# Kernel tuning notes

Measured on AMD Instinct MI355X. Metric: run time of the kernel, lower is better.

The kernel has to match this reference:

```python
import jax, jax.numpy as jnp
import numpy as np

DX = 0.01
DT = 0.5
MU_UP = 0.001

_lap = np.array([[0,0,-1/12,0,0],[0,0,4/3,0,0],[-1/12,4/3,-5,4/3,-1/12],[0,0,4/3,0,0],[0,0,-1/12,0,0]], dtype=np.float32)
_dx = np.array([[0,0,1/12,0,0],[0,0,-8/12,0,0],[0,0,0,0,0],[0,0,8/12,0,0],[0,0,-1/12,0,0]], dtype=np.float32)
K_LAP = jnp.asarray(_lap)[None, None] / (DX * DX)   # [1,1,5,5]
K_DX = jnp.asarray(_dx)[None, None] / DX             # derivative along H axis (torch res_dx)
K_DY = jnp.swapaxes(K_DX, 2, 3)                      # derivative along W axis (torch res_dy)


def _conv(x, k):
    # cross-correlation, VALID, NCHW -- matches torch Conv2d
    return jax.lax.conv_general_dilated(x, k, (1, 1), 'VALID',
                                        dimension_numbers=('NCHW', 'OIHW', 'NCHW'))


def _pad(h):
    # periodic padding of 2 on both spatial dims (torch.cat based circular pad)
    return jnp.pad(h, ((0, 0), (0, 0), (2, 2), (2, 2)), mode='wrap')


def _f_rhs(u, v, Re, UA, UB, VA, VB):
    up, vp = _pad(u), _pad(v)
    u_x, u_y = _conv(up, K_DX), _conv(up, K_DY)
    v_x, v_y = _conv(vp, K_DX), _conv(vp, K_DY)
    nu = MU_UP / Re
    f_u = nu * _conv(up, K_LAP) + UA * u * u_x + UB * v * u_y
    f_v = nu * _conv(vp, K_LAP) + VA * u * v_x + VB * v * v_y
    return f_u, f_v


def setup_inputs() -> dict:
    key = jax.random.key(0)
    k_h, k_re, k_ua, k_ub, k_va, k_vb = jax.random.split(key, 6)
    h = jax.random.normal(k_h, (8, 2, 1024, 1024), dtype=jnp.float32)
    Re = jax.random.uniform(k_re, (), jnp.float32, 0.5, 1.5)  # keep 1/Re well-conditioned
    UA = jax.random.uniform(k_ua, (), jnp.float32)
    UB = jax.random.uniform(k_ub, (), jnp.float32)
    VA = jax.random.uniform(k_va, (), jnp.float32)
    VB = jax.random.uniform(k_vb, (), jnp.float32)
    return {'h': h, 'Re': Re, 'UA': UA, 'UB': UB, 'VA': VA, 'VB': VB}


def reference(h, Re, UA, UB, VA, VB):
    u0 = h[:, 0:1]
    v0 = h[:, 1:2]
    k1u, k1v = _f_rhs(u0, v0, Re, UA, UB, VA, VB)
    k2u, k2v = _f_rhs(u0 + k1u * (DT / 2.0), v0 + k1v * (DT / 2.0), Re, UA, UB, VA, VB)
    k3u, k3v = _f_rhs(u0 + k2u * (DT / 2.0), v0 + k2v * (DT / 2.0), Re, UA, UB, VA, VB)
    k4u, k4v = _f_rhs(u0 + k3u * DT, v0 + k3v * DT, Re, UA, UB, VA, VB)
    u_next = u0 + DT * (k1u + 2 * k2u + 2 * k3u + k4u) / 6.0
    v_next = v0 + DT * (k1v + 2 * k2v + 2 * k3v + k4v) / 6.0
    return jnp.concatenate((u_next, v_next), axis=1)
```

## Files before the change

### kernel.cpp

```cpp
#include <hip/hip_runtime.h>


typedef float f4 __attribute__((ext_vector_type(4)));
typedef float f2 __attribute__((ext_vector_type(2)));

#define LCOLS 100
#define NFLD  8192
#define NT    1024

#define GLOAD16(gp, lp) __builtin_amdgcn_global_load_lds(                      \
    (const __attribute__((address_space(1))) void*)(gp),                       \
    (__attribute__((address_space(3))) void*)(lp), 16, 0, 0)

template<int S>
__device__ __forceinline__ void quad_stage(
    const float* tu, const float* tv, int l,
    float nu, float UA, float UB, float VA, float VB,
    f4& ku, f4& kv, f4& au, f4& av, f4& su, f4& sv, f4& ou, f4& ov)
{
    const float csub = (S==0) ? 0.f : ((S==3) ? 0.5f : 0.25f);
    const float cadd = (S<=1) ? 0.25f : ((S==2) ? 0.5f : 0.f);
    const float wgt  = (S==1 || S==2) ? 2.f : 1.f;
    const float d1 = 800.f/12.f;
    const float d2 = 100.f/12.f;
    const float a1 = (4.f/3.f)*1.0e4f;
    const float a2 = -(1.f/12.f)*1.0e4f;
    const float a0 = -5.0e4f;

    f4 ucc, vcc;
    if (S == 0) { ucc = *(const f4*)(tu+l); vcc = *(const f4*)(tv+l); }
    else        { ucc = su;                 vcc = sv; }
    f2 ul2 = *(const f2*)(tu+l-2);
    f2 ur2 = *(const f2*)(tu+l+4);
    f4 un1 = *(const f4*)(tu+l-LCOLS);
    f4 us1 = *(const f4*)(tu+l+LCOLS);
    f4 un2 = *(const f4*)(tu+l-2*LCOLS);
    f4 us2 = *(const f4*)(tu+l+2*LCOLS);
    f2 vl2 = *(const f2*)(tv+l-2);
    f2 vr2 = *(const f2*)(tv+l+4);
    f4 vn1 = *(const f4*)(tv+l-LCOLS);
    f4 vs1 = *(const f4*)(tv+l+LCOLS);
    f4 vn2 = *(const f4*)(tv+l-2*LCOLS);
    f4 vs2 = *(const f4*)(tv+l+2*LCOLS);
    float hu[8] = {ul2[0],ul2[1],ucc[0],ucc[1],ucc[2],ucc[3],ur2[0],ur2[1]};
    float hv[8] = {vl2[0],vl2[1],vcc[0],vcc[1],vcc[2],vcc[3],vr2[0],vr2[1]};
#pragma unroll
    for (int k = 0; k < 4; ++k) {
        float u = hu[k+2], v = hv[k+2];
        float urow = d1*(us1[k]-un1[k]) + d2*(un2[k]-us2[k]);
        float vrow = d1*(vs1[k]-vn1[k]) + d2*(vn2[k]-vs2[k]);
        float ucol = d1*(hu[k+3]-hu[k+1]) + d2*(hu[k]-hu[k+4]);
        float vcol = d1*(hv[k+3]-hv[k+1]) + d2*(hv[k]-hv[k+4]);
        float ulap = a1*((un1[k]+us1[k])+(hu[k+1]+hu[k+3]))
                   + a2*((un2[k]+us2[k])+(hu[k]+hu[k+4])) + a0*u;
        float vlap = a1*((vn1[k]+vs1[k])+(hv[k+1]+hv[k+3]))
                   + a2*((vn2[k]+vs2[k])+(hv[k]+hv[k+4])) + a0*v;
        float fu = nu*ulap + UA*(u*urow) + UB*(v*ucol);
        float fv = nu*vlap + VA*(u*vrow) + VB*(v*vcol);
        float kuold = ku[k], kvold = kv[k];
        if (S == 3) {
            ou[k] = (u - 0.5f*kuold) + (1.f/12.f)*(au[k] + fu);
            ov[k] = (v - 0.5f*kvold) + (1.f/12.f)*(av[k] + fv);
        } else {
            au[k] += wgt*fu;
            av[k] += wgt*fv;
            su[k] = (u - csub*kuold) + cadd*fu;
            sv[k] = (v - csub*kvold) + cadd*fv;
            ku[k] = fu;
            kv[k] = fv;
        }
    }
}

__global__ __launch_bounds__(NT, 4)
void rk4_stencil(const float* __restrict__ h,
                 const float* __restrict__ sRe, const float* __restrict__ sUA,
                 const float* __restrict__ sUB, const float* __restrict__ sVA,
                 const float* __restrict__ sVB, float* __restrict__ out)
{
    __shared__ __align__(16) float tu[NFLD];
    __shared__ __align__(16) float tv[NFLD];

    const int tid = threadIdx.x;
    const int tc = blockIdx.x, tr = blockIdx.y, bb = blockIdx.z;

    const float Re = sRe[0], UA = sUA[0], UB = sUB[0], VA = sVA[0], VB = sVB[0];
    const float nu = 0.001f / Re;
    const f4 z4 = {0.f, 0.f, 0.f, 0.f};

    const size_t plane = 1048576;
    const float* uin = h + (size_t)(bb*2) * plane;
    const float* vin = uin + plane;
    const int base_r = tr*64 - 8  + 1024;
    const int base_c = tc*64 - 16 + 1024;

    {
        const int wave = tid >> 6, lane = tid & 63;
#pragma unroll
        for (int it = 0; it < 4; ++it) {
            int c = wave + 16*it;
            int fld = (c >= 32);
            int cc  = c & 31;
            int idx = 256*cc + 4*lane;
            int row = idx / LCOLS;
            int col = idx - row*LCOLS;
            int gr = (base_r + row) & 1023;
            int gc = (base_c + col) & 1023;
            const float* gp = (fld ? vin : uin) + ((size_t)gr << 10) + gc;
            float* lp = (fld ? tv : tu) + 256*cc;
            GLOAD16(gp, lp);
        }
    }
    __syncthreads();

    const int wv = tid >> 6, ln = tid & 63;
    const int dqr = 8 + 4*wv + (ln >> 4);
    const int dqc = 4 + (ln & 15);
    const int dl  = dqr*LCOLS + 4*dqc;

    int rqr = 0, rqc = 0;
    if (tid < 496) {
        int i = tid;
        if      (i < 36)  { rqr = 6  + i/18;       rqc = 3 + i%18; }
        else if (i < 72)  { int t=i-36;  rqr = 72 + t/18; rqc = 3 + t%18; }
        else if (i < 136) { rqr = 8 + (i-72);      rqc = 3; }
        else if (i < 200) { rqr = 8 + (i-136);     rqc = 20; }
        else if (i < 236) { int t=i-200; rqr = 4  + t/18; rqc = 3 + t%18; }
        else if (i < 272) { int t=i-236; rqr = 74 + t/18; rqc = 3 + t%18; }
        else if (i < 312) { int t=i-272; rqr = 2  + t/20; rqc = 2 + t%20; }
        else if (i < 352) { int t=i-312; rqr = 76 + t/20; rqc = 2 + t%20; }
        else if (i < 424) { rqr = 4 + (i-352);     rqc = 2; }
        else              { rqr = 4 + (i-424);     rqc = 21; }
    }
    const int rl = rqr*LCOLS + 4*rqc;

    f4 dku=z4, dkv=z4, dau=z4, dav=z4, dsu=z4, dsv=z4;
    f4 rku=z4, rkv=z4, rau=z4, rav=z4, rsu=z4, rsv=z4;
    f4 du0=z4, du1=z4;

    quad_stage<0>(tu,tv,dl, nu,UA,UB,VA,VB, dku,dkv,dau,dav,dsu,dsv, du0,du1);
    if (tid < 496)
        quad_stage<0>(tu,tv,rl, nu,UA,UB,VA,VB, rku,rkv,rau,rav,rsu,rsv, du0,du1);
    __syncthreads();
    *(f4*)(tu+dl) = dsu; *(f4*)(tv+dl) = dsv;
    if (tid < 496) { *(f4*)(tu+rl) = rsu; *(f4*)(tv+rl) = rsv; }
    __syncthreads();

    quad_stage<1>(tu,tv,dl, nu,UA,UB,VA,VB, dku,dkv,dau,dav,dsu,dsv, du0,du1);
    if (tid < 272)
        quad_stage<1>(tu,tv,rl, nu,UA,UB,VA,VB, rku,rkv,rau,rav,rsu,rsv, du0,du1);
    __syncthreads();
    *(f4*)(tu+dl) = dsu; *(f4*)(tv+dl) = dsv;
    if (tid < 272) { *(f4*)(tu+rl) = rsu; *(f4*)(tv+rl) = rsv; }
    __syncthreads();

    quad_stage<2>(tu,tv,dl, nu,UA,UB,VA,VB, dku,dkv,dau,dav,dsu,dsv, du0,du1);
    if (tid < 200)
        quad_stage<2>(tu,tv,rl, nu,UA,UB,VA,VB, rku,rkv,rau,rav,rsu,rsv, du0,du1);
    __syncthreads();
    *(f4*)(tu+dl) = dsu; *(f4*)(tv+dl) = dsv;
    if (tid < 200) { *(f4*)(tu+rl) = rsu; *(f4*)(tv+rl) = rsv; }
    __syncthreads();

    {
        float* outu = out + (size_t)(bb*2) * plane;
        float* outv = outu + plane;
        f4 ou, ov;
        quad_stage<3>(tu,tv,dl, nu,UA,UB,VA,VB, dku,dkv,dau,dav,dsu,dsv, ou,ov);
        int gr = tr*64 + (dqr - 8);
        int gc = tc*64 + 4*dqc - 16;
        *(f4*)(outu + (size_t)gr*1024 + gc) = ou;
        *(f4*)(outv + (size_t)gr*1024 + gc) = ov;
    }
}

extern "C" void kernel_launch(void* const* d_in, const int* in_sizes, int n_in,
                              void* d_out, int out_size, void* d_ws, size_t ws_size,
                              hipStream_t stream) {
    const float* h   = (const float*)d_in[0];
    const float* sRe = (const float*)d_in[1];
    const float* sUA = (const float*)d_in[2];
    const float* sUB = (const float*)d_in[3];
    const float* sVA = (const float*)d_in[4];
    const float* sVB = (const float*)d_in[5];
    float* o = (float*)d_out;
    rk4_stencil<<<dim3(16,16,8), dim3(NT,1,1), 0, stream>>>(h, sRe, sUA, sUB, sVA, sVB, o);
}
```

Before: 211.9 us.

## Halve block size, give each thread two interior quads, skip ring accumulators

After: 351.6 us. 1.66x slower.

```diff
diff --git a/kernel.cpp b/kernel.cpp
--- a/kernel.cpp
+++ b/kernel.cpp
@@ -6,13 +6,13 @@
 
 #define LCOLS 100
 #define NFLD  8192
-#define NT    1024
+#define NT    512
 
 #define GLOAD16(gp, lp) __builtin_amdgcn_global_load_lds(                      \
     (const __attribute__((address_space(1))) void*)(gp),                       \
     (__attribute__((address_space(3))) void*)(lp), 16, 0, 0)
 
-template<int S>
+template<int S, bool ACC>
 __device__ __forceinline__ void quad_stage(
     const float* tu, const float* tv, int l,
     float nu, float UA, float UB, float VA, float VB,
@@ -62,8 +62,10 @@
             ou[k] = (u - 0.5f*kuold) + (1.f/12.f)*(au[k] + fu);
             ov[k] = (v - 0.5f*kvold) + (1.f/12.f)*(av[k] + fv);
         } else {
-            au[k] += wgt*fu;
-            av[k] += wgt*fv;
+            if (ACC) {
+                au[k] += wgt*fu;
+                av[k] += wgt*fv;
+            }
             su[k] = (u - csub*kuold) + cadd*fu;
             sv[k] = (v - csub*kvold) + cadd*fv;
             ku[k] = fu;
@@ -97,8 +99,8 @@
     {
         const int wave = tid >> 6, lane = tid & 63;
 #pragma unroll
-        for (int it = 0; it < 4; ++it) {
-            int c = wave + 16*it;
+        for (int it = 0; it < 8; ++it) {
+            int c = wave + 8*it;
             int fld = (c >= 32);
             int cc  = c & 31;
             int idx = 256*cc + 4*lane;
@@ -114,9 +116,11 @@
     __syncthreads();
 
     const int wv = tid >> 6, ln = tid & 63;
-    const int dqr = 8 + 4*wv + (ln >> 4);
-    const int dqc = 4 + (ln & 15);
-    const int dl  = dqr*LCOLS + 4*dqc;
+    const int dqr0 = 8 + 8*wv + (ln >> 4);
+    const int dqr1 = dqr0 + 4;
+    const int dqc  = 4 + (ln & 15);
+    const int dl0  = dqr0*LCOLS + 4*dqc;
+    const int dl1  = dqr1*LCOLS + 4*dqc;
 
     int rqr = 0, rqc = 0;
     if (tid < 496) {
@@ -134,31 +138,38 @@
     }
     const int rl = rqr*LCOLS + 4*rqc;
 
-    f4 dku=z4, dkv=z4, dau=z4, dav=z4, dsu=z4, dsv=z4;
-    f4 rku=z4, rkv=z4, rau=z4, rav=z4, rsu=z4, rsv=z4;
-    f4 du0=z4, du1=z4;
-
-    quad_stage<0>(tu,tv,dl, nu,UA,UB,VA,VB, dku,dkv,dau,dav,dsu,dsv, du0,du1);
+    f4 dku0=z4, dkv0=z4, dau0=z4, dav0=z4, dsu0=z4, dsv0=z4;
+    f4 dku1=z4, dkv1=z4, dau1=z4, dav1=z4, dsu1=z4, dsv1=z4;
+    f4 rku=z4, rkv=z4, rsu=z4, rsv=z4;
+    f4 dmy0=z4, dmy1=z4;
+
+    quad_stage<0,true >(tu,tv,dl0, nu,UA,UB,VA,VB, dku0,dkv0,dau0,dav0,dsu0,dsv0, dmy0,dmy1);
+    quad_stage<0,true >(tu,tv,dl1, nu,UA,UB,VA,VB, dku1,dkv1,dau1,dav1,dsu1,dsv1, dmy0,dmy1);
     if (tid < 496)
-        quad_stage<0>(tu,tv,rl, nu,UA,UB,VA,VB, rku,rkv,rau,rav,rsu,rsv, du0,du1);
-    __syncthreads();
-    *(f4*)(tu+dl) = dsu; *(f4*)(tv+dl) = dsv;
+        quad_stage<0,false>(tu,tv,rl, nu,UA,UB,VA,VB, rku,rkv,dmy0,dmy1,rsu,rsv, dmy0,dmy1);
+    __syncthreads();
+    *(f4*)(tu+dl0) = dsu0; *(f4*)(tv+dl0) = dsv0;
+    *(f4*)(tu+dl1) = dsu1; *(f4*)(tv+dl1) = dsv1;
     if (tid < 496) { *(f4*)(tu+rl) = rsu; *(f4*)(tv+rl) = rsv; }
     __syncthreads();
 
-    quad_stage<1>(tu,tv,dl, nu,UA,UB,VA,VB, dku,dkv,dau,dav,dsu,dsv, du0,du1);
+    quad_stage<1,true >(tu,tv,dl0, nu,UA,UB,VA,VB, dku0,dkv0,dau0,dav0,dsu0,dsv0, dmy0,dmy1);
+    quad_stage<1,true >(tu,tv,dl1, nu,UA,UB,VA,VB, dku1,dkv1,dau1,dav1,dsu1,dsv1, dmy0,dmy1);
     if (tid < 272)
-        quad_stage<1>(tu,tv,rl, nu,UA,UB,VA,VB, rku,rkv,rau,rav,rsu,rsv, du0,du1);
-    __syncthreads();
-    *(f4*)(tu+dl) = dsu; *(f4*)(tv+dl) = dsv;
+        quad_stage<1,false>(tu,tv,rl, nu,UA,UB,VA,VB, rku,rkv,dmy0,dmy1,rsu,rsv, dmy0,dmy1);
+    __syncthreads();
+    *(f4*)(tu+dl0) = dsu0; *(f4*)(tv+dl0) = dsv0;
+    *(f4*)(tu+dl1) = dsu1; *(f4*)(tv+dl1) = dsv1;
     if (tid < 272) { *(f4*)(tu+rl) = rsu; *(f4*)(tv+rl) = rsv; }
     __syncthreads();
 
-    quad_stage<2>(tu,tv,dl, nu,UA,UB,VA,VB, dku,dkv,dau,dav,dsu,dsv, du0,du1);
+    quad_stage<2,true >(tu,tv,dl0, nu,UA,UB,VA,VB, dku0,dkv0,dau0,dav0,dsu0,dsv0, dmy0,dmy1);
+    quad_stage<2,true >(tu,tv,dl1, nu,UA,UB,VA,VB, dku1,dkv1,dau1,dav1,dsu1,dsv1, dmy0,dmy1);
     if (tid < 200)
-        quad_stage<2>(tu,tv,rl, nu,UA,UB,VA,VB, rku,rkv,rau,rav,rsu,rsv, du0,du1);
-    __syncthreads();
-    *(f4*)(tu+dl) = dsu; *(f4*)(tv+dl) = dsv;
+        quad_stage<2,false>(tu,tv,rl, nu,UA,UB,VA,VB, rku,rkv,dmy0,dmy1,rsu,rsv, dmy0,dmy1);
+    __syncthreads();
+    *(f4*)(tu+dl0) = dsu0; *(f4*)(tv+dl0) = dsv0;
+    *(f4*)(tu+dl1) = dsu1; *(f4*)(tv+dl1) = dsv1;
     if (tid < 200) { *(f4*)(tu+rl) = rsu; *(f4*)(tv+rl) = rsv; }
     __syncthreads();
 
@@ -166,11 +177,15 @@
         float* outu = out + (size_t)(bb*2) * plane;
         float* outv = outu + plane;
         f4 ou, ov;
-        quad_stage<3>(tu,tv,dl, nu,UA,UB,VA,VB, dku,dkv,dau,dav,dsu,dsv, ou,ov);
-        int gr = tr*64 + (dqr - 8);
-        int gc = tc*64 + 4*dqc - 16;
-        *(f4*)(outu + (size_t)gr*1024 + gc) = ou;
-        *(f4*)(outv + (size_t)gr*1024 + gc) = ov;
+        const int gc = tc*64 + 4*dqc - 16;
+        quad_stage<3,true>(tu,tv,dl0, nu,UA,UB,VA,VB, dku0,dkv0,dau0,dav0,dsu0,dsv0, ou,ov);
+        int gr0 = tr*64 + (dqr0 - 8);
+        *(f4*)(outu + (size_t)gr0*1024 + gc) = ou;
+        *(f4*)(outv + (size_t)gr0*1024 + gc) = ov;
+        quad_stage<3,true>(tu,tv,dl1, nu,UA,UB,VA,VB, dku1,dkv1,dau1,dav1,dsu1,dsv1, ou,ov);
+        int gr1 = tr*64 + (dqr1 - 8);
+        *(f4*)(outu + (size_t)gr1*1024 + gc) = ou;
+        *(f4*)(outv + (size_t)gr1*1024 + gc) = ov;
     }
 }
 
```
